# Performance work log

Hardware: AMD Instinct MI355X
Metric: run time of the kernel (lower is better)

The kernel has to match this reference:

```python
import jax, jax.numpy as jnp
import numpy as np

B, N, D = 8, 2048, 768
K, H, G = 256, 12, 4
DH = D // H          # 64
EPS = 1e-12


def grouped_pointwise(x, w):
    """Grouped Conv1d with kernel_size=1, no bias.
    x: (b, n, d); w: (g, out_per_g, in_per_g) [torch weight (d, d/g, 1) reshaped].
    """
    b, n, d = x.shape
    g = w.shape[0]
    xg = x.reshape(b, n, g, d // g)
    return jnp.einsum('bngi,goi->bngo', xg, w).reshape(b, n, d)


def setup_inputs() -> dict:
    key = jax.random.key(0)
    ks = jax.random.split(key, 8)
    std_conv = 1.0 / np.sqrt(D // G)   # torch conv default ~ U(-sqrt(1/fan_in), ...)
    std_pk = 1.0 / np.sqrt(K)          # init_ uses last dim of (seq_len, k_dim)
    std_lin = 1.0 / np.sqrt(D)
    return {
        'input_embedding': jax.random.normal(ks[0], (B, N, D), jnp.float32),
        'wq': jax.random.uniform(ks[1], (G, D // G, D // G), jnp.float32, -std_conv, std_conv),
        'wk': jax.random.uniform(ks[2], (G, D // G, D // G), jnp.float32, -std_conv, std_conv),
        'project_k': jax.random.uniform(ks[3], (N, K), jnp.float32, -std_pk, std_pk),
        'w_out': jax.random.uniform(ks[4], (D, D), jnp.float32, -std_lin, std_lin),
        'b_out': jax.random.uniform(ks[5], (D,), jnp.float32, -std_lin, std_lin),
        'gamma': jnp.ones((D,), jnp.float32),
        'beta': jnp.zeros((D,), jnp.float32),
    }


def reference(input_embedding, wq, wk, project_k, w_out, b_out, gamma, beta):
    x = input_embedding                       # (b, n, d)
    b, n, d = x.shape

    queries = grouped_pointwise(x, wq)        # (b, n, d)
    k_raw = grouped_pointwise(x, wk)          # (b, n, d)  (key conv)
    k_proj = jnp.einsum('bnd,nk->bkd', k_raw, project_k)   # (b, K, d)

    # Faithful replication of: keys.permute(0,2,1).view(b, K, h, dh)
    # (memory-reinterpreting reshape of the (b, d, K) layout)
    keys = jnp.transpose(k_proj, (0, 2, 1)).reshape(b, K, H, DH)
    keys = jnp.transpose(keys, (0, 2, 1, 3))                # (b, h, K, dh)

    # values also come from the key conv (self.value unused in source forward)
    values = k_proj.reshape(b, K, H, DH).transpose(0, 2, 1, 3)   # (b, h, K, dh)
    q = queries.reshape(b, n, H, DH).transpose(0, 2, 1, 3)       # (b, h, n, dh)

    dots = jnp.einsum('bhnd,bhkd->bhnk', q, keys) / np.sqrt(DH)
    attn = jax.nn.softmax(dots, axis=-1)      # dropout = identity (eval)
    ctx = jnp.einsum('bhnk,bhkd->bhnd', attn, values)
    ctx = ctx.transpose(0, 2, 1, 3).reshape(b, n, d)

    out = ctx @ w_out.T + b_out               # nn.Linear
    y = x + out                               # residual
    mu = jnp.mean(y, axis=-1, keepdims=True)
    var = jnp.mean((y - mu) ** 2, axis=-1, keepdims=True)
    return (y - mu) / jnp.sqrt(var + EPS) * gamma + beta
```

## Files before the change

### kernel.cpp

```cpp
#include <hip/hip_runtime.h>
#include <hip/hip_bf16.h>

typedef short short8 __attribute__((ext_vector_type(8)));
typedef short short4v __attribute__((ext_vector_type(4)));
typedef int i32x4 __attribute__((ext_vector_type(4)));
typedef float f32x4 __attribute__((ext_vector_type(4)));

#define MFMA(a, b, c) __builtin_amdgcn_mfma_f32_16x16x32_bf16((a), (b), (c), 0, 0, 0)

__device__ __forceinline__ short f2bf(float f) {
  unsigned u = __builtin_bit_cast(unsigned, f);
  unsigned r = u + 0x7FFFu + ((u >> 16) & 1u);
  return (short)(r >> 16);
}

__device__ __forceinline__ float bf2f(short s) {
  unsigned u = ((unsigned)(unsigned short)s) << 16;
  return __builtin_bit_cast(float, u);
}

__device__ __forceinline__ short8 cvt8(float4 a, float4 b) {
  short8 t;
  t[0] = f2bf(a.x); t[1] = f2bf(a.y); t[2] = f2bf(a.z); t[3] = f2bf(a.w);
  t[4] = f2bf(b.x); t[5] = f2bf(b.y); t[6] = f2bf(b.z); t[7] = f2bf(b.w);
  return t;
}

__global__ __launch_bounds__(256) void k_prep(
    const float* __restrict__ wq, const float* __restrict__ wk,
    const float* __restrict__ wout, const float* __restrict__ pk,
    short* __restrict__ wqb, short* __restrict__ wkb,
    short* __restrict__ woutb, short* __restrict__ pkT)
{
  int idx = blockIdx.x * 256 + threadIdx.x;
  if (idx < 147456) { wqb[idx] = f2bf(wq[idx]); wkb[idx] = f2bf(wk[idx]); }
  if (idx < 589824) { woutb[idx] = f2bf(wout[idx]); }
  if (idx < 524288) {
    int n = idx >> 8, k = idx & 255;
    pkT[(size_t)k * 2048 + n] = f2bf(pk[idx]);
  }
}

__global__ __launch_bounds__(256, 2) void k_conv(
    const float* __restrict__ x, const short* __restrict__ wqb,
    short* __restrict__ qo, short* __restrict__ xbT)
{
  __shared__ __align__(16) short Xs[64 * 192];
  const int tid = threadIdx.x, lane = tid & 63, w = tid >> 6;
  const int g = blockIdx.y;
  const int m0 = blockIdx.x * 64;
  const int wr = (w >> 1) * 32, wcol = (w & 1) * 96;
  const int lrow = lane & 15, g4 = lane >> 4, lk8 = g4 * 8;

  {
    const int r = tid >> 2, cb = (tid & 3) * 48;
    const int sw = (r ^ (r >> 3)) & 7;
    const float* src = x + (size_t)(m0 + r) * 768 + g * 192 + cb;
#pragma unroll
    for (int i = 0; i < 6; i++) {
      float4 v0 = *(const float4*)(src + i * 8);
      float4 v1 = *(const float4*)(src + i * 8 + 4);
      int o = (cb >> 3) + i;
      *(short8*)&Xs[r * 192 + ((o ^ sw) << 3)] = cvt8(v0, v1);
    }
  }
  __syncthreads();

  f32x4 acc[2][6];
#pragma unroll
  for (int mi = 0; mi < 2; mi++)
#pragma unroll
    for (int cf = 0; cf < 6; cf++) acc[mi][cf] = (f32x4)0.f;

  const int row0 = wr + lrow, row1 = wr + 16 + lrow;
  const int sw0 = (row0 ^ (row0 >> 3)) & 7;
  const int sw1 = (row1 ^ (row1 >> 3)) & 7;

#pragma unroll
  for (int s = 0; s < 6; s++) {
    const int k0 = s * 32;
    const int ob = (k0 >> 3) + g4;
    short8 a0 = *(const short8*)&Xs[row0 * 192 + ((ob ^ sw0) << 3)];
    short8 a1 = *(const short8*)&Xs[row1 * 192 + ((ob ^ sw1) << 3)];
#pragma unroll
    for (int cf = 0; cf < 6; cf++) {
      short8 bb = *(const short8*)(wqb + ((size_t)g * 192 + wcol + cf * 16 + lrow) * 192 + k0 + lk8);
      acc[0][cf] = MFMA(a0, bb, acc[0][cf]);
      acc[1][cf] = MFMA(a1, bb, acc[1][cf]);
    }
  }

#pragma unroll
  for (int mi = 0; mi < 2; mi++)
#pragma unroll
    for (int cf = 0; cf < 6; cf++)
#pragma unroll
      for (int j = 0; j < 4; j++) {
        int m = m0 + wr + mi * 16 + g4 * 4 + j;
        qo[(size_t)m * 768 + g * 192 + wcol + cf * 16 + lrow] = f2bf(acc[mi][cf][j]);
      }

  {
    const int b = m0 >> 11, n0 = m0 & 2047;
    const int el = tid >> 3, oct = tid & 7;
#pragma unroll
    for (int ec = 0; ec < 6; ec++) {
      const int c = ec * 32 + el;
      const int o = c >> 3, ci = c & 7;
      short8 v;
#pragma unroll
      for (int u = 0; u < 8; u++) {
        const int n = oct * 8 + u;
        v[u] = Xs[n * 192 + (((o ^ (u ^ oct)) << 3)) + ci];
      }
      *(short8*)(xbT + ((size_t)b * 768 + g * 192 + c) * 2048 + n0 + oct * 8) = v;
    }
  }
}

__global__ __launch_bounds__(512, 4) void k_xproj(
    const short* __restrict__ pkT, const short* __restrict__ xbT,
    float* __restrict__ xproj)
{
  __shared__ __align__(16) short A2[2][64][72];
  __shared__ __align__(16) short B2[2][64][72];
  const int tid = threadIdx.x, lane = tid & 63, w = tid >> 6;
  const int f = blockIdx.x;
  const int xcd = f & 7, rem = f >> 3;
  const int k2t4 = rem & 3, eb8 = rem >> 2;
  const int e_b = eb8 * 8 + xcd;
  const int k2t = k2t4 * 64;
  const int et = (e_b % 12) * 64, b = e_b / 12;
  const int lrow = lane & 15, g4 = lane >> 4, lk8 = g4 * 8;
  const int wa = (w & 3) * 16, wb = (w >> 2) * 32;

  const int r = tid >> 3, c8 = tid & 7;
  const short* aSrc = pkT + (size_t)(k2t + r) * 2048 + c8 * 8;
  const short* bSrc = xbT + ((size_t)b * 768 + et + r) * 2048 + c8 * 8;

  {
    short8 gA = *(const short8*)aSrc;
    short8 gB = *(const short8*)bSrc;
    *(short8*)&A2[0][r][c8 * 8] = gA;
    *(short8*)&B2[0][r][c8 * 8] = gB;
  }
  __syncthreads();

  f32x4 acc[2];
  acc[0] = (f32x4)0.f; acc[1] = (f32x4)0.f;

  short8 gA, gB;
#pragma unroll 2
  for (int t = 0; t < 32; ++t) {
    const int cur = t & 1;
    if (t < 31) {
      gA = *(const short8*)(aSrc + (t + 1) * 64);
      gB = *(const short8*)(bSrc + (t + 1) * 64);
    }
    short8 af0 = *(const short8*)&A2[cur][wa + lrow][lk8];
    short8 af1 = *(const short8*)&A2[cur][wa + lrow][32 + lk8];
    short8 bf00 = *(const short8*)&B2[cur][wb + lrow][lk8];
    short8 bf01 = *(const short8*)&B2[cur][wb + lrow][32 + lk8];
    short8 bf10 = *(const short8*)&B2[cur][wb + 16 + lrow][lk8];
    short8 bf11 = *(const short8*)&B2[cur][wb + 16 + lrow][32 + lk8];
    acc[0] = MFMA(af0, bf00, acc[0]);
    acc[0] = MFMA(af1, bf01, acc[0]);
    acc[1] = MFMA(af0, bf10, acc[1]);
    acc[1] = MFMA(af1, bf11, acc[1]);
    if (t < 31) {
      *(short8*)&A2[cur ^ 1][r][c8 * 8] = gA;
      *(short8*)&B2[cur ^ 1][r][c8 * 8] = gB;
    }
    __syncthreads();
  }

  float* dst = xproj + ((size_t)b * 256 + k2t + wa) * 768 + et + wb;
#pragma unroll
  for (int cf = 0; cf < 2; cf++)
#pragma unroll
    for (int j = 0; j < 4; j++)
      dst[(size_t)(g4 * 4 + j) * 768 + cf * 16 + lrow] = acc[cf][j];
}

__global__ __launch_bounds__(256) void k_kconv(
    float* xpio, const short* __restrict__ wkb)
{
  const int tid = threadIdx.x, lane = tid & 63, w = tid >> 6;
  const int rt = blockIdx.x * 64, g = blockIdx.y, b = blockIdx.z;
  const int wr = (w >> 1) * 32, wcol = (w & 1) * 96;
  const int lrow = lane & 15, g4 = lane >> 4, lk8 = (lane >> 4) * 8;

  f32x4 acc[2][6];
#pragma unroll
  for (int mi = 0; mi < 2; mi++)
#pragma unroll
    for (int cf = 0; cf < 6; cf++) acc[mi][cf] = (f32x4)0.f;

#pragma unroll
  for (int s = 0; s < 6; s++) {
    int k0 = s * 32;
    short8 af[2];
#pragma unroll
    for (int mi = 0; mi < 2; mi++) {
      const float* ap = xpio + ((size_t)b * 256 + rt + wr + mi * 16 + lrow) * 768
                        + g * 192 + k0 + lk8;
      float4 f0 = *(const float4*)ap;
      float4 f1 = *(const float4*)(ap + 4);
      af[mi] = cvt8(f0, f1);
    }
#pragma unroll
    for (int cf = 0; cf < 6; cf++) {
      short8 bb = *(const short8*)(wkb + ((size_t)g * 192 + wcol + cf * 16 + lrow) * 192 + k0 + lk8);
      acc[0][cf] = MFMA(af[0], bb, acc[0][cf]);
      acc[1][cf] = MFMA(af[1], bb, acc[1][cf]);
    }
  }
  __syncthreads();
#pragma unroll
  for (int mi = 0; mi < 2; mi++)
#pragma unroll
    for (int cf = 0; cf < 6; cf++)
#pragma unroll
      for (int j = 0; j < 4; j++) {
        int k2 = rt + wr + mi * 16 + g4 * 4 + j;
        xpio[((size_t)b * 256 + k2) * 768 + g * 192 + wcol + cf * 16 + lrow] =
            acc[mi][cf][j];
      }
}

__global__ __launch_bounds__(256) void k_gather(
    const float* __restrict__ kp, short* __restrict__ Kb, short* __restrict__ Vb)
{
  const int h = blockIdx.x, b = blockIdx.y;
  const int bh = b * 12 + h;
  const int tid = threadIdx.x;
  const float* kpb = kp + (size_t)b * 196608;
  {
    const int kb4 = (h & 3) * 64, doff = h >> 2;
    const int dh = tid & 63, kq = tid >> 6;
    const float* row = kpb + (size_t)(kb4 + dh) * 768 + doff;
    short* dst = Kb + (size_t)bh * 18432 + dh;
#pragma unroll 8
    for (int i = 0; i < 64; i++) {
      int k2 = kq * 64 + i;
      dst[(size_t)k2 * 72] = f2bf(row[3 * k2]);
    }
  }
  {
    short* dst = Vb + (size_t)bh * 16384;
#pragma unroll
    for (int i = 0; i < 8; i++) {
      int oct = tid + 256 * i;
      int k2h = oct >> 6, dh = oct & 63;
      short8 v;
#pragma unroll
      for (int u = 0; u < 8; u++)
        v[u] = f2bf(kpb[(size_t)(k2h * 8 + u) * 768 + h * 64 + dh]);
      *(short8*)&dst[oct * 8] = v;
    }
  }
}

__global__ __launch_bounds__(512, 4) void k_attn(
    const short* __restrict__ qws, const short* __restrict__ Kb,
    const short* __restrict__ Vb, short* __restrict__ ctx)
{
  __shared__ __align__(16) short Kls[18432];
  __shared__ __align__(16) short Vls[16384];
  const int tid = threadIdx.x, lane = tid & 63, w = tid >> 6;
  const int n0 = blockIdx.x * 128;
  const int h = blockIdx.y, b = blockIdx.z;
  const int bh = b * 12 + h;

  {
    const short8* gk = (const short8*)(Kb + (size_t)bh * 18432);
    short8* lk = (short8*)Kls;
#pragma unroll
    for (int i = 0; i < 4; i++) lk[tid + 512 * i] = gk[tid + 512 * i];
    if (tid < 256) lk[tid + 2048] = gk[tid + 2048];
    const short8* gv = (const short8*)(Vb + (size_t)bh * 16384);
    short8* lv = (short8*)Vls;
#pragma unroll
    for (int i = 0; i < 4; i++) lv[tid + 512 * i] = gv[tid + 512 * i];
  }
  const int lrow = lane & 15, g = lane >> 4, lk8 = g * 8;
  const int nrow = n0 + w * 16;
  const short* qp = qws + ((size_t)b * 2048 + nrow + lrow) * 768 + h * 64;
  short8 bq0 = *(const short8*)(qp + lk8);
  short8 bq1 = *(const short8*)(qp + 32 + lk8);
  __syncthreads();

  f32x4 s[16];
#pragma unroll
  for (int fc = 0; fc < 16; fc++) s[fc] = (f32x4)0.f;
  __builtin_amdgcn_s_setprio(1);
#pragma unroll
  for (int fc = 0; fc < 16; fc++) {
    short8 ak0 = *(const short8*)&Kls[(fc * 16 + lrow) * 72 + lk8];
    short8 ak1 = *(const short8*)&Kls[(fc * 16 + lrow) * 72 + 32 + lk8];
    s[fc] = MFMA(ak0, bq0, s[fc]);
    s[fc] = MFMA(ak1, bq1, s[fc]);
  }
  __builtin_amdgcn_s_setprio(0);

  float mx = -3.0e38f;
#pragma unroll
  for (int fc = 0; fc < 16; fc++)
#pragma unroll
    for (int j = 0; j < 4; j++) mx = fmaxf(mx, s[fc][j]);
  mx = fmaxf(mx, __shfl_xor(mx, 16));
  mx = fmaxf(mx, __shfl_xor(mx, 32));
  float sum = 0.f;
#pragma unroll
  for (int fc = 0; fc < 16; fc++)
#pragma unroll
    for (int j = 0; j < 4; j++) {
      float e = __expf(0.125f * (s[fc][j] - mx));
      s[fc][j] = e; sum += e;
    }
  sum += __shfl_xor(sum, 16);
  sum += __shfl_xor(sum, 32);
  float inv = 1.f / sum;

  unsigned pku[16][2];
#pragma unroll
  for (int fc = 0; fc < 16; fc++) {
    pku[fc][0] = (unsigned)(unsigned short)f2bf(s[fc][0] * inv)
               | ((unsigned)(unsigned short)f2bf(s[fc][1] * inv) << 16);
    pku[fc][1] = (unsigned)(unsigned short)f2bf(s[fc][2] * inv)
               | ((unsigned)(unsigned short)f2bf(s[fc][3] * inv) << 16);
  }

  f32x4 o[4];
#pragma unroll
  for (int fd = 0; fd < 4; fd++) o[fd] = (f32x4)0.f;
  const int L0 = ((lane & 16) << 1) + lrow;
  const int L1 = L0 + 16;
  const bool hi = (lane >= 32);
  __builtin_amdgcn_s_setprio(1);
#pragma unroll
  for (int t = 0; t < 8; t++) {
    unsigned a0 = (unsigned)__shfl((int)pku[2 * t][0], L0);
    unsigned a1 = (unsigned)__shfl((int)pku[2 * t][1], L0);
    unsigned a2 = (unsigned)__shfl((int)pku[2 * t][0], L1);
    unsigned a3 = (unsigned)__shfl((int)pku[2 * t][1], L1);
    unsigned c0 = (unsigned)__shfl((int)pku[2 * t + 1][0], L0);
    unsigned c1 = (unsigned)__shfl((int)pku[2 * t + 1][1], L0);
    unsigned c2 = (unsigned)__shfl((int)pku[2 * t + 1][0], L1);
    unsigned c3 = (unsigned)__shfl((int)pku[2 * t + 1][1], L1);
    i32x4 bi = { (int)(hi ? c0 : a0), (int)(hi ? c1 : a1),
                 (int)(hi ? c2 : a2), (int)(hi ? c3 : a3) };
    short8 bfrag = __builtin_bit_cast(short8, bi);
#pragma unroll
    for (int fd = 0; fd < 4; fd++) {
      short8 av = *(const short8*)&Vls[((t * 4 + g) * 64 + fd * 16 + lrow) * 8];
      o[fd] = MFMA(av, bfrag, o[fd]);
    }
  }
  __builtin_amdgcn_s_setprio(0);
#pragma unroll
  for (int fd = 0; fd < 4; fd++) {
    short4v st;
#pragma unroll
    for (int j = 0; j < 4; j++) st[j] = f2bf(o[fd][j]);
    *(short4v*)&ctx[((size_t)b * 2048 + n0 + w * 16 + lrow) * 768
                    + h * 64 + fd * 16 + 4 * g] = st;
  }
}

__global__ __launch_bounds__(512, 2) void k_gemm_yln(
    const short* __restrict__ ctx, const short* __restrict__ woutb,
    const float* __restrict__ bout, const float* __restrict__ x,
    const float* __restrict__ gamma, const float* __restrict__ beta,
    float* __restrict__ out)
{
  __shared__ __align__(16) short As[64][40];
  __shared__ __align__(16) short Bs[768][40];
  const int tid = threadIdx.x, lane = tid & 63, w = tid >> 6;
  const int m0 = blockIdx.x * 64;
  const int lrow = lane & 15, g4 = lane >> 4, lk8 = g4 * 8;
  const int wr = w >> 1;
  const int wc = w & 1;
  const int colbase = wc * 384;

  const int rb = tid >> 2, c8 = (tid & 3) * 8;
  const short* aSrc = ctx + (size_t)(m0 + rb) * 768 + c8;
  const short* bSrc = woutb + (size_t)rb * 768 + c8;

  {
    if (tid < 256) *(short8*)&As[rb][c8] = *(const short8*)aSrc;
#pragma unroll
    for (int i = 0; i < 6; i++)
      *(short8*)&Bs[rb + 128 * i][c8] = *(const short8*)(bSrc + (size_t)i * 98304);
  }
  __syncthreads();

  f32x4 acc[24];
#pragma unroll
  for (int cf = 0; cf < 24; cf++) acc[cf] = (f32x4)0.f;

  short8 pA;
  short8 pB[6];
#pragma unroll 2
  for (int t = 0; t < 24; ++t) {
    if (t < 23) {
      if (tid < 256) pA = *(const short8*)(aSrc + (t + 1) * 32);
#pragma unroll
      for (int i = 0; i < 6; i++)
        pB[i] = *(const short8*)(bSrc + (size_t)i * 98304 + (t + 1) * 32);
    }
    short8 af = *(const short8*)&As[wr * 16 + lrow][lk8];
#pragma unroll
    for (int cf = 0; cf < 24; cf++) {
      short8 bf = *(const short8*)&Bs[colbase + cf * 16 + lrow][lk8];
      acc[cf] = MFMA(af, bf, acc[cf]);
    }
    __syncthreads();
    if (t < 23) {
      if (tid < 256) *(short8*)&As[rb][c8] = pA;
#pragma unroll
      for (int i = 0; i < 6; i++)
        *(short8*)&Bs[rb + 128 * i][c8] = pB[i];
    }
    __syncthreads();
  }

  float s1[4] = {0.f, 0.f, 0.f, 0.f}, s2[4] = {0.f, 0.f, 0.f, 0.f};
#pragma unroll
  for (int cf = 0; cf < 24; cf++) {
    const int col = colbase + cf * 16 + lrow;
    float bb = bout[col];
#pragma unroll
    for (int j = 0; j < 4; j++) {
      const int row = m0 + wr * 16 + g4 * 4 + j;
      float yv = acc[cf][j] + bb + x[(size_t)row * 768 + col];
      acc[cf][j] = yv;
      s1[j] += yv; s2[j] += yv * yv;
    }
  }
#pragma unroll
  for (int m = 1; m < 16; m <<= 1) {
#pragma unroll
    for (int j = 0; j < 4; j++) {
      s1[j] += __shfl_xor(s1[j], m);
      s2[j] += __shfl_xor(s2[j], m);
    }
  }
  float2* red = (float2*)&As[0][0];
  if (lrow == 0) {
#pragma unroll
    for (int j = 0; j < 4; j++) {
      float2 t; t.x = s1[j]; t.y = s2[j];
      red[wc * 64 + wr * 16 + g4 * 4 + j] = t;
    }
  }
  __syncthreads();
  float mean_[4], rstd_[4];
#pragma unroll
  for (int j = 0; j < 4; j++) {
    const int rl = wr * 16 + g4 * 4 + j;
    float2 p0 = red[rl], p1 = red[64 + rl];
    float S1 = p0.x + p1.x, S2 = p0.y + p1.y;
    float mu = S1 * (1.f / 768.f);
    float var = S2 * (1.f / 768.f) - mu * mu;
    mean_[j] = mu;
    rstd_[j] = rsqrtf(var + 1e-12f);
  }
#pragma unroll
  for (int cf = 0; cf < 24; cf++) {
    const int col = colbase + cf * 16 + lrow;
    float gm = gamma[col], bt = beta[col];
#pragma unroll
    for (int j = 0; j < 4; j++) {
      const int row = m0 + wr * 16 + g4 * 4 + j;
      out[(size_t)row * 768 + col] = (acc[cf][j] - mean_[j]) * rstd_[j] * gm + bt;
    }
  }
}

extern "C" void kernel_launch(void* const* d_in, const int* in_sizes, int n_in,
                              void* d_out, int out_size, void* d_ws, size_t ws_size,
                              hipStream_t stream)
{
  const float* x     = (const float*)d_in[0];
  const float* wq    = (const float*)d_in[1];
  const float* wk    = (const float*)d_in[2];
  const float* pk    = (const float*)d_in[3];
  const float* wout  = (const float*)d_in[4];
  const float* bout  = (const float*)d_in[5];
  const float* gamma = (const float*)d_in[6];
  const float* beta  = (const float*)d_in[7];
  float* out = (float*)d_out;

  char* ws = (char*)d_ws;
  short* qbf   = (short*)(ws + 0);
  short* xbT   = (short*)(ws + 25165824);
  float* kpbuf = (float*)(ws + 50331648);
  short* wqb   = (short*)(ws + 56623104);
  short* wkb   = (short*)(ws + 56918016);
  short* woutb = (short*)(ws + 57212928);
  short* pkT   = (short*)(ws + 58392576);
  if (ws_size < 59441152) return;
  short* ctx = (short*)xbT;

  short* Kb = (short*)d_out;
  short* Vb = Kb + 96 * 18432;

  k_prep<<<2304, 256, 0, stream>>>(wq, wk, wout, pk, wqb, wkb, woutb, pkT);
  k_conv<<<dim3(256, 4), 256, 0, stream>>>(x, wqb, qbf, xbT);
  k_xproj<<<384, 512, 0, stream>>>(pkT, xbT, kpbuf);
  k_kconv<<<dim3(4, 4, 8), 256, 0, stream>>>(kpbuf, wkb);
  k_gather<<<dim3(12, 8), 256, 0, stream>>>(kpbuf, Kb, Vb);
  k_attn<<<dim3(16, 12, 8), 512, 0, stream>>>(qbf, Kb, Vb, ctx);
  k_gemm_yln<<<256, 512, 0, stream>>>(ctx, woutb, bout, x, gamma, beta, out);
}
```

Baseline: 169.9 us.

## Restructure output GEMM+LayerNorm with double-buffered direct-to-LDS loads and 4x6 wave tiles

Rewrites the out-projection GEMM fused with residual and LayerNorm. Operands now go straight from global memory into double-buffered LDS via global_load_lds, so only one barrier per k-step is needed instead of register staging with two barriers. Each wave now owns all 64 rows and a 96-column slice (a 4x6 MFMA tile), which raises fragment reuse per LDS read. The row-statistics reduction now combines partials from 8 waves through LDS. The unpadded 32-short LDS rows may cause bank conflicts, and the larger accumulator array raises register pressure.

```diff
diff --git a/kernel.cpp b/kernel.cpp
--- a/kernel.cpp
+++ b/kernel.cpp
@@ -24,6 +24,12 @@
   t[0] = f2bf(a.x); t[1] = f2bf(a.y); t[2] = f2bf(a.z); t[3] = f2bf(a.w);
   t[4] = f2bf(b.x); t[5] = f2bf(b.y); t[6] = f2bf(b.z); t[7] = f2bf(b.w);
   return t;
+}
+
+__device__ __forceinline__ void gl2lds16(const void* g, void* l) {
+  __builtin_amdgcn_global_load_lds(
+      (const __attribute__((address_space(1))) void*)g,
+      (__attribute__((address_space(3))) void*)l, 16, 0, 0);
 }
 
 __global__ __launch_bounds__(256) void k_prep(
@@ -96,7 +102,7 @@
     for (int cf = 0; cf < 6; cf++)
 #pragma unroll
       for (int j = 0; j < 4; j++) {
-        int m = m0 + wr + mi * 16 + g4 * 4 + j;
+        int m = m0 + wr + mi * 16 + (lane >> 4) * 4 + j;
         qo[(size_t)m * 768 + g * 192 + wcol + cf * 16 + lrow] = f2bf(acc[mi][cf][j]);
       }
 
@@ -374,108 +380,124 @@
     const float* __restrict__ gamma, const float* __restrict__ beta,
     float* __restrict__ out)
 {
-  __shared__ __align__(16) short As[64][40];
-  __shared__ __align__(16) short Bs[768][40];
+  __shared__ __align__(16) short As[2][64][32];
+  __shared__ __align__(16) short Bs[2][768][32];
+  __shared__ float2 mr[64];
   const int tid = threadIdx.x, lane = tid & 63, w = tid >> 6;
   const int m0 = blockIdx.x * 64;
   const int lrow = lane & 15, g4 = lane >> 4, lk8 = g4 * 8;
-  const int wr = w >> 1;
-  const int wc = w & 1;
-  const int colbase = wc * 384;
-
-  const int rb = tid >> 2, c8 = (tid & 3) * 8;
-  const short* aSrc = ctx + (size_t)(m0 + rb) * 768 + c8;
-  const short* bSrc = woutb + (size_t)rb * 768 + c8;
-
-  {
-    if (tid < 256) *(short8*)&As[rb][c8] = *(const short8*)aSrc;
-#pragma unroll
-    for (int i = 0; i < 6; i++)
-      *(short8*)&Bs[rb + 128 * i][c8] = *(const short8*)(bSrc + (size_t)i * 98304);
-  }
-  __syncthreads();
-
-  f32x4 acc[24];
-#pragma unroll
-  for (int cf = 0; cf < 24; cf++) acc[cf] = (f32x4)0.f;
-
-  short8 pA;
-  short8 pB[6];
-#pragma unroll 2
+  const int colbase = w * 96;
+
+  const int srow = lane >> 2;
+  const int sk8 = (lane & 3) * 8;
+  const short* bSrc = woutb + (size_t)(w * 16 + srow) * 768 + sk8;
+  const short* aSrc = ctx + (size_t)(m0 + (w & 3) * 16 + srow) * 768 + sk8;
+
+#define STAGE_YLN(buf, t)                                                     \
+  do {                                                                        \
+    _Pragma("unroll")                                                         \
+    for (int i_ = 0; i_ < 6; i_++)                                            \
+      gl2lds16(bSrc + (size_t)i_ * 98304 + (t) * 32,                          \
+               &Bs[buf][i_ * 128 + w * 16][0]);                               \
+    if (w < 4)                                                                \
+      gl2lds16(aSrc + (t) * 32, &As[buf][w * 16][0]);                         \
+  } while (0)
+
+  STAGE_YLN(0, 0);
+  __syncthreads();
+
+  f32x4 acc[4][6];
+#pragma unroll
+  for (int rf = 0; rf < 4; rf++)
+#pragma unroll
+    for (int cf = 0; cf < 6; cf++) acc[rf][cf] = (f32x4)0.f;
+
   for (int t = 0; t < 24; ++t) {
-    if (t < 23) {
-      if (tid < 256) pA = *(const short8*)(aSrc + (t + 1) * 32);
-#pragma unroll
-      for (int i = 0; i < 6; i++)
-        pB[i] = *(const short8*)(bSrc + (size_t)i * 98304 + (t + 1) * 32);
-    }
-    short8 af = *(const short8*)&As[wr * 16 + lrow][lk8];
-#pragma unroll
-    for (int cf = 0; cf < 24; cf++) {
-      short8 bf = *(const short8*)&Bs[colbase + cf * 16 + lrow][lk8];
-      acc[cf] = MFMA(af, bf, acc[cf]);
-    }
+    const int cur = t & 1;
+    if (t < 23) STAGE_YLN(cur ^ 1, t + 1);
+    short8 af[4], bf[6];
+#pragma unroll
+    for (int rf = 0; rf < 4; rf++)
+      af[rf] = *(const short8*)&As[cur][rf * 16 + lrow][lk8];
+#pragma unroll
+    for (int cf = 0; cf < 6; cf++)
+      bf[cf] = *(const short8*)&Bs[cur][colbase + cf * 16 + lrow][lk8];
+#pragma unroll
+    for (int rf = 0; rf < 4; rf++)
+#pragma unroll
+      for (int cf = 0; cf < 6; cf++)
+        acc[rf][cf] = MFMA(af[rf], bf[cf], acc[rf][cf]);
     __syncthreads();
-    if (t < 23) {
-      if (tid < 256) *(short8*)&As[rb][c8] = pA;
-#pragma unroll
-      for (int i = 0; i < 6; i++)
-        *(short8*)&Bs[rb + 128 * i][c8] = pB[i];
-    }
-    __syncthreads();
-  }
-
-  float s1[4] = {0.f, 0.f, 0.f, 0.f}, s2[4] = {0.f, 0.f, 0.f, 0.f};
-#pragma unroll
-  for (int cf = 0; cf < 24; cf++) {
-    const int col = colbase + cf * 16 + lrow;
-    float bb = bout[col];
-#pragma unroll
-    for (int j = 0; j < 4; j++) {
-      const int row = m0 + wr * 16 + g4 * 4 + j;
-      float yv = acc[cf][j] + bb + x[(size_t)row * 768 + col];
-      acc[cf][j] = yv;
-      s1[j] += yv; s2[j] += yv * yv;
-    }
-  }
-#pragma unroll
-  for (int m = 1; m < 16; m <<= 1) {
-#pragma unroll
-    for (int j = 0; j < 4; j++) {
-      s1[j] += __shfl_xor(s1[j], m);
-      s2[j] += __shfl_xor(s2[j], m);
-    }
-  }
-  float2* red = (float2*)&As[0][0];
+  }
+
+  float bb[6];
+#pragma unroll
+  for (int cf = 0; cf < 6; cf++) bb[cf] = bout[colbase + cf * 16 + lrow];
+
+  float p1[4][4], p2[4][4];
+#pragma unroll
+  for (int rf = 0; rf < 4; rf++)
+#pragma unroll
+    for (int j = 0; j < 4; j++) { p1[rf][j] = 0.f; p2[rf][j] = 0.f; }
+
+#pragma unroll
+  for (int rf = 0; rf < 4; rf++)
+#pragma unroll
+    for (int cf = 0; cf < 6; cf++)
+#pragma unroll
+      for (int j = 0; j < 4; j++) {
+        const int row = m0 + rf * 16 + g4 * 4 + j;
+        const int col = colbase + cf * 16 + lrow;
+        float yv = acc[rf][cf][j] + bb[cf] + x[(size_t)row * 768 + col];
+        acc[rf][cf][j] = yv;
+        p1[rf][j] += yv; p2[rf][j] += yv * yv;
+      }
+#pragma unroll
+  for (int m = 1; m < 16; m <<= 1)
+#pragma unroll
+    for (int rf = 0; rf < 4; rf++)
+#pragma unroll
+      for (int j = 0; j < 4; j++) {
+        p1[rf][j] += __shfl_xor(p1[rf][j], m);
+        p2[rf][j] += __shfl_xor(p2[rf][j], m);
+      }
+  float2* red = (float2*)&As[0][0][0];
   if (lrow == 0) {
 #pragma unroll
-    for (int j = 0; j < 4; j++) {
-      float2 t; t.x = s1[j]; t.y = s2[j];
-      red[wc * 64 + wr * 16 + g4 * 4 + j] = t;
-    }
-  }
-  __syncthreads();
-  float mean_[4], rstd_[4];
-#pragma unroll
-  for (int j = 0; j < 4; j++) {
-    const int rl = wr * 16 + g4 * 4 + j;
-    float2 p0 = red[rl], p1 = red[64 + rl];
-    float S1 = p0.x + p1.x, S2 = p0.y + p1.y;
+    for (int rf = 0; rf < 4; rf++)
+#pragma unroll
+      for (int j = 0; j < 4; j++) {
+        float2 tp; tp.x = p1[rf][j]; tp.y = p2[rf][j];
+        red[(rf * 16 + g4 * 4 + j) * 8 + w] = tp;
+      }
+  }
+  __syncthreads();
+  if (tid < 64) {
+    float S1 = 0.f, S2 = 0.f;
+#pragma unroll
+    for (int i = 0; i < 8; i++) {
+      float2 p = red[tid * 8 + i];
+      S1 += p.x; S2 += p.y;
+    }
     float mu = S1 * (1.f / 768.f);
     float var = S2 * (1.f / 768.f) - mu * mu;
-    mean_[j] = mu;
-    rstd_[j] = rsqrtf(var + 1e-12f);
-  }
-#pragma unroll
-  for (int cf = 0; cf < 24; cf++) {
-    const int col = colbase + cf * 16 + lrow;
-    float gm = gamma[col], bt = beta[col];
-#pragma unroll
-    for (int j = 0; j < 4; j++) {
-      const int row = m0 + wr * 16 + g4 * 4 + j;
-      out[(size_t)row * 768 + col] = (acc[cf][j] - mean_[j]) * rstd_[j] * gm + bt;
-    }
-  }
+    float2 t2; t2.x = mu; t2.y = rsqrtf(var + 1e-12f);
+    mr[tid] = t2;
+  }
+  __syncthreads();
+#pragma unroll
+  for (int rf = 0; rf < 4; rf++)
+#pragma unroll
+    for (int cf = 0; cf < 6; cf++) {
+      const int col = colbase + cf * 16 + lrow;
+      float gm = gamma[col], bt = beta[col];
+#pragma unroll
+      for (int j = 0; j < 4; j++) {
+        const int row = m0 + rf * 16 + g4 * 4 + j;
+        float2 ms = mr[rf * 16 + g4 * 4 + j];
+        out[(size_t)row * 768 + col] = (acc[rf][cf][j] - ms.x) * ms.y * gm + bt;
+      }
+    }
 }
 
 extern "C" void kernel_launch(void* const* d_in, const int* in_sizes, int n_in,
```

Measured after the change: 166.9 us. About the same (-1.8%).
